# Kernel optimization log

Measured on AMD Instinct MI355X. Metric: run time of the kernel, lower is better.

Reference implementation:

```python
import jax, jax.numpy as jnp
import numpy as np

C_S, C_P, C_H, H, P_QK, P_V = 384, 128, 16, 12, 4, 8
B, N = 1, 512
INF = 1e5
EPS = 1e-8


def quat_to_rot(q):
    w, x, y, z = q[..., 0], q[..., 1], q[..., 2], q[..., 3]
    return jnp.stack([
        jnp.stack([1 - 2 * (y * y + z * z), 2 * (x * y - w * z), 2 * (x * z + w * y)], -1),
        jnp.stack([2 * (x * y + w * z), 1 - 2 * (x * x + z * z), 2 * (y * z - w * x)], -1),
        jnp.stack([2 * (x * z - w * y), 2 * (y * z + w * x), 1 - 2 * (x * x + y * y)], -1),
    ], -2)


def layer_norm(x, g, b):
    m = x.mean(-1, keepdims=True)
    v = ((x - m) ** 2).mean(-1, keepdims=True)
    return (x - m) * jax.lax.rsqrt(v + 1e-5) * g + b


def setup_inputs():
    key = jax.random.key(0)
    ks = iter(jax.random.split(key, 64))

    def w(shape, scale=0.02):
        return jax.random.normal(next(ks), shape, dtype=jnp.float32) * scale

    inp = {}
    inp['s'] = jax.random.normal(next(ks), (B, N, C_S), dtype=jnp.float32)
    inp['p'] = jax.random.normal(next(ks), (B, N, N, C_P), dtype=jnp.float32)
    q = jax.random.normal(next(ks), (B, N, 4), dtype=jnp.float32)
    inp['rot'] = quat_to_rot(q / jnp.linalg.norm(q, axis=-1, keepdims=True))
    inp['trans'] = jax.random.normal(next(ks), (B, N, 3), dtype=jnp.float32)
    inp['mask'] = jnp.ones((B, N), dtype=jnp.float32)
    inp['w_q'] = w((C_S, H * C_H)); inp['b_q'] = jnp.zeros((H * C_H,), jnp.float32)
    inp['w_kv'] = w((C_S, 2 * H * C_H)); inp['b_kv'] = jnp.zeros((2 * H * C_H,), jnp.float32)
    inp['w_qp'] = w((C_S, H * P_QK * 3)); inp['b_qp'] = jnp.zeros((H * P_QK * 3,), jnp.float32)
    inp['w_kvp'] = w((C_S, H * (P_QK + P_V) * 3)); inp['b_kvp'] = jnp.zeros((H * (P_QK + P_V) * 3,), jnp.float32)
    inp['w_b'] = w((C_P, H)); inp['b_b'] = jnp.zeros((H,), jnp.float32)
    inp['head_w'] = w((H,), 0.5)
    d_out = H * (C_H + C_P + P_V * 4)  # 2112
    inp['w_o'] = w((d_out, C_S)); inp['b_o'] = jnp.zeros((C_S,), jnp.float32)
    inp['ln1_g'] = jnp.ones((C_S,), jnp.float32); inp['ln1_b'] = jnp.zeros((C_S,), jnp.float32)
    for i in (1, 2, 3):
        inp['tw%d' % i] = w((C_S, C_S)); inp['tb%d' % i] = jnp.zeros((C_S,), jnp.float32)
    inp['ln2_g'] = jnp.ones((C_S,), jnp.float32); inp['ln2_b'] = jnp.zeros((C_S,), jnp.float32)
    inp['bb_w'] = w((C_S, 6)); inp['bb_b'] = jnp.zeros((6,), jnp.float32)
    return inp


def forward(s, p, rot, trans, mask, w_q, b_q, w_kv, b_kv, w_qp, b_qp, w_kvp, b_kvp,
            w_b, b_b, head_w, w_o, b_o, ln1_g, ln1_b,
            tw1, tb1, tw2, tb2, tw3, tb3, ln2_g, ln2_b, bb_w, bb_b):
    # ---- Invariant Point Attention ----
    q = (s @ w_q + b_q).reshape(B, N, H, C_H)
    k, v = jnp.split((s @ w_kv + b_kv).reshape(B, N, H, 2 * C_H), 2, axis=-1)
    qp = (s @ w_qp + b_qp).reshape(B, N, H * P_QK, 3)
    qp = (jnp.einsum('bnij,bnpj->bnpi', rot, qp) + trans[:, :, None, :]).reshape(B, N, H, P_QK, 3)
    kvp = (s @ w_kvp + b_kvp).reshape(B, N, H * (P_QK + P_V), 3)
    kvp = (jnp.einsum('bnij,bnpj->bnpi', rot, kvp) + trans[:, :, None, :]).reshape(B, N, H, P_QK + P_V, 3)
    kp, vp = kvp[..., :P_QK, :], kvp[..., P_QK:, :]
    bias = p @ w_b + b_b  # [B,N,N,H]
    a = jnp.einsum('bihc,bjhc->bhij', q, k) * float(np.sqrt(1.0 / (3 * C_H)))
    a = a + float(np.sqrt(1.0 / 3)) * jnp.transpose(bias, (0, 3, 1, 2))
    d2 = ((qp[:, :, None] - kp[:, None]) ** 2).sum(-1)  # [B,N,N,H,Pqk]
    hw = jax.nn.softplus(head_w) * float(np.sqrt(1.0 / (3 * (P_QK * 9.0 / 2))))
    pt_att = -0.5 * (d2 * hw[:, None]).sum(-1)  # [B,N,N,H]
    sq_mask = (mask[:, :, None] * mask[:, None, :] - 1.0) * INF  # [B,N,N]
    a = jax.nn.softmax(a + jnp.transpose(pt_att, (0, 3, 1, 2)) + sq_mask[:, None], axis=-1)
    o = jnp.einsum('bhij,bjhc->bihc', a, v).reshape(B, N, H * C_H)
    op = jnp.einsum('bhij,bjhpc->bihpc', a, vp) - trans[:, :, None, None, :]
    op = jnp.einsum('bnji,bnhpj->bnhpi', rot, op)  # invert-apply frames
    op_norm = jnp.sqrt((op ** 2).sum(-1) + EPS)  # [B,N,H,Pv]
    o_pair = jnp.einsum('bhij,bijc->bihc', a, p).reshape(B, N, H * C_P)
    cat = jnp.concatenate([o, op.reshape(B, N, H * P_V * 3), op_norm.reshape(B, N, H * P_V), o_pair], -1)
    s = s + cat @ w_o + b_o
    s = layer_norm(s, ln1_g, ln1_b)
    # ---- structure transition (1 layer, residual + LN) ----
    h = jax.nn.relu(s @ tw1 + tb1)
    h = jax.nn.relu(h @ tw2 + tb2)
    s = layer_norm(s + h @ tw3 + tb3, ln2_g, ln2_b)
    # ---- backbone update + frame compose ----
    upd = s @ bb_w + bb_b  # [B,N,6]
    quat = jnp.concatenate([jnp.ones((B, N, 1), s.dtype), upd[..., :3]], -1)
    quat = quat / jnp.linalg.norm(quat, axis=-1, keepdims=True)
    r_u = quat_to_rot(quat)
    rot_new = jnp.einsum('bnij,bnjk->bnik', rot, r_u)
    trans_new = jnp.einsum('bnij,bnj->bni', rot, upd[..., 3:]) + trans
    return s, rot_new, trans_new


def reference(s, p, rot, trans, mask, w_q, b_q, w_kv, b_kv, w_qp, b_qp, w_kvp, b_kvp,
              w_b, b_b, head_w, w_o, b_o, ln1_g, ln1_b,
              tw1, tb1, tw2, tb2, tw3, tb3, ln2_g, ln2_b, bb_w, bb_b):
    return forward(s, p, rot, trans, mask, w_q, b_q, w_kv, b_kv, w_qp, b_qp, w_kvp, b_kvp,
                   w_b, b_b, head_w, w_o, b_o, ln1_g, ln1_b,
                   tw1, tb1, tw2, tb2, tw3, tb3, ln2_g, ln2_b, bb_w, bb_b)
```

## Files before the change

### kernel.cpp

```cpp
#include <hip/hip_runtime.h>
#include <math.h>

#define N 512
#define CS 384
#define CP 128
#define CH 16
#define NH 12
#define NN (N*N)
#define DCAT 2112
#define INFV 100000.0f

__device__ __constant__ float SC_QK = 0.14433756729740643f;
#define SC_B  0.57735026918962576f
#define HW_SC 0.13608276348795434f

typedef __attribute__((ext_vector_type(8))) short bf16x8;
typedef __attribute__((ext_vector_type(4))) float f32x4;
typedef __attribute__((ext_vector_type(4))) short sh4;
typedef __attribute__((ext_vector_type(4))) unsigned u32x4;
typedef unsigned short ushort_t;

__device__ inline short f2bf(float v) {
    unsigned u = __builtin_bit_cast(unsigned, v);
    u += 0x7FFF + ((u >> 16) & 1);
    return (short)(u >> 16);
}
__device__ inline float bf2f(ushort_t u) {
    unsigned x = ((unsigned)u) << 16;
    return __builtin_bit_cast(float, x);
}
__device__ __forceinline__ unsigned cvtpk(float a, float b) {
    unsigned r;
    asm("v_cvt_pk_bf16_f32 %0, %1, %2" : "=v"(r) : "v"(a), "v"(b));
    return r;
}

__device__ __forceinline__ void gload16(const void* g, void* l) {
    __builtin_amdgcn_global_load_lds(
        (const __attribute__((address_space(1))) unsigned int*)g,
        (__attribute__((address_space(3))) unsigned int*)l,
        16, 0, 0);
}

struct PrepArgs {
    const float* wsrc0; const float* wsrc1; const float* wsrc2; const float* wsrc3;
    const float* wsrc4; const float* wsrc5; const float* wsrc6; const float* wsrc7;
    ushort_t* wdst0; ushort_t* wdst1; ushort_t* wdst2; ushort_t* wdst3;
    ushort_t* wdst4; ushort_t* wdst5; ushort_t* wdst6; ushort_t* wdst7;
    const float* s; ushort_t* sbf;
    const float* bq; const float* bkv; const float* bqp; const float* bkvp;
    float* biasp;
};

__global__ __launch_bounds__(256) void prep_kernel(PrepArgs a)
{
    const int b = blockIdx.x;
    if (b < 1668) {
        const float* src; ushort_t* dst; int begin, nx, Nc, K;
        if      (b < 72)   { src=a.wsrc0; dst=a.wdst0; begin=0;    nx=6;  Nc=192; K=384; }
        else if (b < 216)  { src=a.wsrc1; dst=a.wdst1; begin=72;   nx=12; Nc=384; K=384; }
        else if (b < 276)  { src=a.wsrc2; dst=a.wdst2; begin=216;  nx=5;  Nc=144; K=384; }
        else if (b < 444)  { src=a.wsrc3; dst=a.wdst3; begin=276;  nx=14; Nc=432; K=384; }
        else if (b < 1236) { src=a.wsrc4; dst=a.wdst4; begin=444;  nx=12; Nc=384; K=2112; }
        else if (b < 1380) { src=a.wsrc5; dst=a.wdst5; begin=1236; nx=12; Nc=384; K=384; }
        else if (b < 1524) { src=a.wsrc6; dst=a.wdst6; begin=1380; nx=12; Nc=384; K=384; }
        else               { src=a.wsrc7; dst=a.wdst7; begin=1524; nx=12; Nc=384; K=384; }
        int lb = b - begin;
        int cx = (lb % nx) * 32, ky = (lb / nx) * 32;
        __shared__ float tile[32][33];
        const int tx = threadIdx.x & 31, ty = threadIdx.x >> 5;
        for (int r = ty; r < 32; r += 8) {
            int c = cx + tx;
            tile[r][tx] = (c < Nc) ? src[(size_t)(ky + r) * Nc + c] : 0.f;
        }
        __syncthreads();
        for (int r = ty; r < 32; r += 8) {
            int orow = cx + r;
            if (orow < Nc)
                dst[(size_t)orow * K + ky + tx] = (ushort_t)f2bf(tile[tx][r]);
        }
    } else if (b < 1860) {
        int i4 = (b - 1668) * 256 + threadIdx.x;
        f32x4 v = *(const f32x4*)(a.s + (size_t)i4 * 4);
        sh4 o;
        o[0] = f2bf(v[0]); o[1] = f2bf(v[1]); o[2] = f2bf(v[2]); o[3] = f2bf(v[3]);
        *(sh4*)(a.sbf + (size_t)i4 * 4) = o;
    } else {
        for (int idx = threadIdx.x; idx < 1152; idx += 256) {
            float v;
            if (idx < 192)      v = a.bq[idx];
            else if (idx < 576) v = a.bkv[idx - 192];
            else if (idx < 720) v = a.bqp[idx - 576];
            else                v = a.bkvp[idx - 720];
            a.biasp[idx] = v;
        }
    }
}

__global__ __launch_bounds__(256) void gemm_bf16(
    const ushort_t* __restrict__ A, const ushort_t* __restrict__ Bt,
    float* __restrict__ part, int K, int KOUT, int nk)
{
    __shared__ __align__(16) ushort_t As[2][2048];
    __shared__ __align__(16) ushort_t Bs[2][2048];
    const int t = threadIdx.x, w = t >> 6, l = t & 63;
    const int i0 = blockIdx.x * 64, n0 = blockIdx.y * 64, sp = blockIdx.z;
    const int kbase = sp * nk * 32;

    const int srow = w * 16 + (l >> 2);
    const int skb = (l & 3) ^ ((srow >> 1) & 3);
    const ushort_t* aSrc = A + (size_t)(i0 + srow) * K + kbase + skb * 8;
    const ushort_t* bSrc = Bt + (size_t)(n0 + srow) * K + kbase + skb * 8;
    ushort_t* aDst = &As[0][0] + w * 512;
    ushort_t* bDst = &Bs[0][0] + w * 512;

    const int r0 = (w >> 1) * 32, c0 = (w & 1) * 32, lr = l & 15, hk = l >> 4;
    int aOff[2], bOff[2];
    #pragma unroll
    for (int m = 0; m < 2; ++m) {
        int row = r0 + m * 16 + lr;
        aOff[m] = row * 64 + ((hk ^ ((row >> 1) & 3)) << 4);
    }
    #pragma unroll
    for (int n = 0; n < 2; ++n) {
        int row = c0 + n * 16 + lr;
        bOff[n] = row * 64 + ((hk ^ ((row >> 1) & 3)) << 4);
    }

    f32x4 acc[2][2];
    #pragma unroll
    for (int m = 0; m < 2; ++m)
        #pragma unroll
        for (int n = 0; n < 2; ++n) acc[m][n] = (f32x4){0.f, 0.f, 0.f, 0.f};

    gload16(aSrc, aDst);
    gload16(bSrc, bDst);
    __syncthreads();

    int cur = 0;
    for (int it = 0; it < nk; ++it) {
        if (it + 1 < nk) {
            gload16(aSrc + (it + 1) * 32, aDst + (cur ^ 1) * 2048);
            gload16(bSrc + (it + 1) * 32, bDst + (cur ^ 1) * 2048);
        }
        const char* ab = (const char*)&As[cur][0];
        const char* bb = (const char*)&Bs[cur][0];
        bf16x8 a0 = *(const bf16x8*)(ab + aOff[0]);
        bf16x8 a1 = *(const bf16x8*)(ab + aOff[1]);
        bf16x8 b0 = *(const bf16x8*)(bb + bOff[0]);
        bf16x8 b1 = *(const bf16x8*)(bb + bOff[1]);
        acc[0][0] = __builtin_amdgcn_mfma_f32_16x16x32_bf16(a0, b0, acc[0][0], 0, 0, 0);
        acc[0][1] = __builtin_amdgcn_mfma_f32_16x16x32_bf16(a0, b1, acc[0][1], 0, 0, 0);
        acc[1][0] = __builtin_amdgcn_mfma_f32_16x16x32_bf16(a1, b0, acc[1][0], 0, 0, 0);
        acc[1][1] = __builtin_amdgcn_mfma_f32_16x16x32_bf16(a1, b1, acc[1][1], 0, 0, 0);
        __syncthreads();
        cur ^= 1;
    }

    #pragma unroll
    for (int m = 0; m < 2; ++m)
        #pragma unroll
        for (int n = 0; n < 2; ++n) {
            int col = n0 + c0 + n * 16 + lr;
            int rowb = i0 + r0 + m * 16 + (l >> 4) * 4;
            float* pr = part + ((size_t)sp * 512 + rowb) * KOUT + col;
            #pragma unroll
            for (int j = 0; j < 4; ++j)
                pr[(size_t)j * KOUT] = acc[m][n][j];
        }
}

__global__ void reduce_k(const float* __restrict__ parts, int S, int KOUT,
                         const float* __restrict__ bias, const float* __restrict__ resid,
                         int relu, float* __restrict__ outf, ushort_t* __restrict__ outbf)
{
    int i4 = blockIdx.x * 256 + threadIdx.x;
    int tot = 512 * KOUT / 4;
    if (i4 >= tot) return;
    int idx = i4 * 4, c = idx % KOUT;
    f32x4 v = *(const f32x4*)(bias + c);
    for (int s2 = 0; s2 < S; ++s2)
        v += *(const f32x4*)(parts + (size_t)s2 * 512 * KOUT + idx);
    if (resid) v += *(const f32x4*)(resid + idx);
    if (relu) {
        v[0] = fmaxf(v[0], 0.f); v[1] = fmaxf(v[1], 0.f);
        v[2] = fmaxf(v[2], 0.f); v[3] = fmaxf(v[3], 0.f);
    }
    if (outf) *(f32x4*)(outf + idx) = v;
    if (outbf) {
        sh4 o;
        o[0] = f2bf(v[0]); o[1] = f2bf(v[1]); o[2] = f2bf(v[2]); o[3] = f2bf(v[3]);
        *(sh4*)(outbf + idx) = o;
    }
}

__global__ void reduce_ln(const float* __restrict__ parts, int S,
                          const float* __restrict__ gbias, const float* __restrict__ resid,
                          const float* __restrict__ g, const float* __restrict__ b,
                          float* __restrict__ outf, ushort_t* __restrict__ outbf,
                          const float* __restrict__ bb_w, const float* __restrict__ bb_b,
                          const float* __restrict__ rot, const float* __restrict__ trans,
                          float* __restrict__ out_rot, float* __restrict__ out_trans)
{
    __shared__ float buf[384];
    __shared__ float red[2], red2[2];
    __shared__ float ush[2][6];
    const int i = blockIdx.x, t = threadIdx.x;
    float s = 0.f, sq = 0.f;
    for (int k = t; k < 384; k += 128) {
        float v = gbias[k] + resid[(size_t)i * 384 + k];
        for (int s2 = 0; s2 < S; ++s2)
            v += parts[((size_t)s2 * 512 + i) * 384 + k];
        buf[k] = v; s += v; sq += v * v;
    }
    for (int off = 32; off; off >>= 1) { s += __shfl_xor(s, off); sq += __shfl_xor(sq, off); }
    if ((t & 63) == 0) { red[t >> 6] = s; red2[t >> 6] = sq; }
    __syncthreads();
    float mean = (red[0] + red[1]) * (1.0f / 384.0f);
    float var = (red2[0] + red2[1]) * (1.0f / 384.0f) - mean * mean;
    float rstd = rsqrtf(var + 1e-5f);
    float onorm[3];
    #pragma unroll
    for (int kk = 0; kk < 3; ++kk) {
        int k = t + kk * 128;
        float o = (buf[k] - mean) * rstd * g[k] + b[k];
        onorm[kk] = o;
        if (outf) outf[(size_t)i * 384 + k] = o;
        if (outbf) outbf[(size_t)i * 384 + k] = (ushort_t)f2bf(o);
    }
    if (!bb_w) return;
    float u[6] = {0.f, 0.f, 0.f, 0.f, 0.f, 0.f};
    #pragma unroll
    for (int kk = 0; kk < 3; ++kk) {
        int k = t + kk * 128;
        float sv = onorm[kk];
        #pragma unroll
        for (int c = 0; c < 6; ++c) u[c] += sv * bb_w[k * 6 + c];
    }
    #pragma unroll
    for (int c = 0; c < 6; ++c)
        for (int off = 32; off; off >>= 1) u[c] += __shfl_xor(u[c], off);
    if ((t & 63) == 0) {
        #pragma unroll
        for (int c = 0; c < 6; ++c) ush[t >> 6][c] = u[c];
    }
    __syncthreads();
    if (t == 0) {
        float uu[6];
        #pragma unroll
        for (int c = 0; c < 6; ++c) uu[c] = ush[0][c] + ush[1][c] + bb_b[c];
        float inq = rsqrtf(1.0f + uu[0]*uu[0] + uu[1]*uu[1] + uu[2]*uu[2]);
        float w = inq, x = uu[0]*inq, y = uu[1]*inq, z = uu[2]*inq;
        float Ru[9];
        Ru[0] = 1.f - 2.f*(y*y + z*z); Ru[1] = 2.f*(x*y - w*z); Ru[2] = 2.f*(x*z + w*y);
        Ru[3] = 2.f*(x*y + w*z); Ru[4] = 1.f - 2.f*(x*x + z*z); Ru[5] = 2.f*(y*z - w*x);
        Ru[6] = 2.f*(x*z - w*y); Ru[7] = 2.f*(y*z + w*x); Ru[8] = 1.f - 2.f*(x*x + y*y);
        const float* R = rot + i * 9;
        #pragma unroll
        for (int a = 0; a < 3; ++a) {
            #pragma unroll
            for (int cc = 0; cc < 3; ++cc)
                out_rot[i * 9 + a * 3 + cc] =
                    R[a*3+0]*Ru[0+cc] + R[a*3+1]*Ru[3+cc] + R[a*3+2]*Ru[6+cc];
            out_trans[i * 3 + a] = R[a*3+0]*uu[3] + R[a*3+1]*uu[4] + R[a*3+2]*uu[5]
                                   + trans[i * 3 + a];
        }
    }
}

__global__ __launch_bounds__(256) void postproj_kernel(
    const float* __restrict__ parts, const float* __restrict__ biasp,
    const float* __restrict__ rot, const float* __restrict__ trans,
    const float* __restrict__ head_w, const float* __restrict__ mask,
    ushort_t* __restrict__ Qext, ushort_t* __restrict__ Kext, ushort_t* __restrict__ Vext)
{
    __shared__ float buf[1152];
    __shared__ float hwv[12], kc28[12];
    const int j = blockIdx.x, t = threadIdx.x;
    for (int c = t; c < 1152; c += 256)
        buf[c] = biasp[c] + parts[(size_t)j * 1152 + c] + parts[(size_t)(512 + j) * 1152 + c];
    if (t >= 192 && t < 204) {
        int h = t - 192;
        hwv[h] = HW_SC * log1pf(expf(head_w[h]));
    }
    __syncthreads();
    if (t < 192) {
        int base = 576 + t * 3;
        const float* R = rot + j * 9;
        const float* T = trans + j * 3;
        float x = buf[base], y = buf[base + 1], z = buf[base + 2];
        float nx = R[0]*x + R[1]*y + R[2]*z + T[0];
        float ny = R[3]*x + R[4]*y + R[5]*z + T[1];
        float nz = R[6]*x + R[7]*y + R[8]*z + T[2];
        buf[base] = nx; buf[base + 1] = ny; buf[base + 2] = nz;
    }
    __syncthreads();
    if (t < 12) {
        float s2 = 0.f;
        #pragma unroll
        for (int e = 0; e < 12; ++e) { float v = buf[720 + t * 36 + e]; s2 += v * v; }
        kc28[t] = -0.5f * hwv[t] * s2 + (mask[j] - 1.0f) * INFV;
    }
    __syncthreads();
    if (t < 192) {
        int h = t >> 4, c0 = (t & 15) * 2;
        float hwf = hwv[h];
        #pragma unroll
        for (int e = 0; e < 2; ++e) {
            int c = c0 + e;
            float qv, kv2;
            if (c < 16)      { qv = SC_QK * buf[h * 16 + c];           kv2 = buf[192 + h * 32 + c]; }
            else if (c < 28) { qv = hwf * buf[576 + h * 12 + (c - 16)]; kv2 = buf[720 + h * 36 + (c - 16)]; }
            else if (c == 28){ qv = 1.f;                               kv2 = kc28[h]; }
            else             { qv = 0.f;                               kv2 = 0.f; }
            Qext[(size_t)h * 16384 + j * 32 + c] = (ushort_t)f2bf(qv);
            Kext[(size_t)h * 16384 + j * 32 + c] = (ushort_t)f2bf(kv2);
        }
    }
    for (int idx = t; idx < 576; idx += 256) {
        int h = idx / 48, c = idx % 48;
        float v;
        if (c < 16)      v = buf[192 + h * 32 + 16 + c];
        else if (c < 40) v = buf[720 + h * 36 + 12 + (c - 16)];
        else             v = 0.f;
        Vext[(size_t)h * 24576 + c * 512 + j] = (ushort_t)f2bf(v);
    }
}

__global__ __launch_bounds__(256) void bias_mfma(
    const float* __restrict__ p, const float* __restrict__ w_b,
    const float* __restrict__ b_b, ushort_t* __restrict__ bias_b)
{
    __shared__ __align__(16) float Pf[64 * 128];
    __shared__ __align__(16) ushort_t Wbs[16 * 128];
    const int t = threadIdx.x, w = t >> 6;
    const size_t row0 = (size_t)blockIdx.x * 64;

    for (int idx = t; idx < 2048; idx += 256) {
        int h = idx >> 7, c = idx & 127;
        float v = (h < 12) ? w_b[c * 12 + h] : 0.f;
        int byte = h * 256 + ((c * 2) ^ ((h & 7) << 4));
        *(ushort_t*)((char*)Wbs + byte) = (ushort_t)f2bf(v);
    }
    #pragma unroll
    for (int k = 0; k < 8; ++k) {
        int s = k * 256 + t;
        int row = s >> 5, ch = s & 31;
        const char* src = (const char*)(p + (row0 + row) * 128) + ((ch ^ (row & 7)) * 16);
        gload16(src, (char*)Pf + (size_t)(k * 256 + w * 64) * 16);
    }
    __syncthreads();

    const int l = t & 63, lr = l & 15, hk = l >> 4;
    const int jb = w * 16;
    f32x4 acc = (f32x4){0.f, 0.f, 0.f, 0.f};
    #pragma unroll
    for (int ks = 0; ks < 4; ++ks) {
        int row = jb + lr;
        int kc = ks * 8 + hk * 2;
        const char* base = (const char*)Pf + row * 512;
        f32x4 v0 = *(const f32x4*)(base + ((kc ^ (row & 7)) * 16));
        f32x4 v1 = *(const f32x4*)(base + (((kc + 1) ^ (row & 7)) * 16));
        bf16x8 afr;
        afr[0] = f2bf(v0[0]); afr[1] = f2bf(v0[1]); afr[2] = f2bf(v0[2]); afr[3] = f2bf(v0[3]);
        afr[4] = f2bf(v1[0]); afr[5] = f2bf(v1[1]); afr[6] = f2bf(v1[2]); afr[7] = f2bf(v1[3]);
        bf16x8 bfr = *(const bf16x8*)((char*)Wbs + lr * 256 +
                        ((ks * 64 + hk * 16) ^ ((lr & 7) << 4)));
        acc = __builtin_amdgcn_mfma_f32_16x16x32_bf16(afr, bfr, acc, 0, 0, 0);
    }
    if (lr < 12) {
        float bb = b_b[lr];
        size_t gj = row0 + jb + hk * 4;
        sh4 o;
        #pragma unroll
        for (int r = 0; r < 4; ++r) o[r] = f2bf(SC_B * (acc[r] + bb));
        *(sh4*)(bias_b + (size_t)lr * NN + gj) = o;
    }
}

__global__ __launch_bounds__(256) void attn_mfma(
    const ushort_t* __restrict__ Qext, const ushort_t* __restrict__ Kext,
    const ushort_t* __restrict__ bias_b, const ushort_t* __restrict__ Vext,
    const float* __restrict__ rot, const float* __restrict__ trans,
    ushort_t* __restrict__ attn_b, ushort_t* __restrict__ catb)
{
    __shared__ float sc[16 * 516];
    __shared__ float redm[64];
    __shared__ float invr[16];
    __shared__ float opl[16][25];
    const int t = threadIdx.x, w = t >> 6, l = t & 63;
    const int i0 = blockIdx.x * 16, h = blockIdx.y;
    const int lr = l & 15, hk = l >> 4;

    #pragma unroll
    for (int it = 0; it < 8; ++it) {
        int elem = (t + it * 256) * 4;
        int i = elem >> 9, j = elem & 511;
        sh4 raw = *(const sh4*)(bias_b + (size_t)h * NN + (size_t)(i0 + i) * 512 + j);
        f32x4 v;
        v[0] = bf2f((ushort_t)raw[0]); v[1] = bf2f((ushort_t)raw[1]);
        v[2] = bf2f((ushort_t)raw[2]); v[3] = bf2f((ushort_t)raw[3]);
        *(f32x4*)(sc + i * 516 + j) = v;
    }
    __syncthreads();

    bf16x8 a0 = *(const bf16x8*)(Qext + (size_t)h * 16384 + (i0 + lr) * 32 + hk * 8);
    f32x4 acc[8];
    #pragma unroll
    for (int n = 0; n < 8; ++n) {
        bf16x8 b = *(const bf16x8*)(Kext + (size_t)h * 16384 +
                                    (w * 128 + n * 16 + lr) * 32 + hk * 8);
        acc[n] = __builtin_amdgcn_mfma_f32_16x16x32_bf16(a0, b, (f32x4){0.f,0.f,0.f,0.f}, 0, 0, 0);
    }

    float rmax[4] = {-3.0e38f, -3.0e38f, -3.0e38f, -3.0e38f};
    #pragma unroll
    for (int n = 0; n < 8; ++n) {
        int col = w * 128 + n * 16 + lr;
        #pragma unroll
        for (int r = 0; r < 4; ++r) {
            int row = hk * 4 + r;
            float v = acc[n][r] + sc[row * 516 + col];
            sc[row * 516 + col] = v;
            rmax[r] = fmaxf(rmax[r], v);
        }
    }
    #pragma unroll
    for (int r = 0; r < 4; ++r) {
        float v = rmax[r];
        v = fmaxf(v, __shfl_xor(v, 1));
        v = fmaxf(v, __shfl_xor(v, 2));
        v = fmaxf(v, __shfl_xor(v, 4));
        v = fmaxf(v, __shfl_xor(v, 8));
        if (lr == 0) redm[w * 16 + hk * 4 + r] = v;
    }
    __syncthreads();

    {
        int row = t >> 4, g = t & 15;
        float mx = fmaxf(fmaxf(redm[row], redm[16 + row]),
                         fmaxf(redm[32 + row], redm[48 + row]));
        float sum = 0.f;
        float* sr = sc + row * 516;
        for (int c = g; c < 512; c += 16) {
            float e = expf(sr[c] - mx);
            sr[c] = e;
            sum += e;
        }
        sum += __shfl_xor(sum, 1);
        sum += __shfl_xor(sum, 2);
        sum += __shfl_xor(sum, 4);
        sum += __shfl_xor(sum, 8);
        if (g == 0) invr[row] = 1.0f / sum;
    }
    __syncthreads();

    #pragma unroll
    for (int it = 0; it < 8; ++it) {
        int elem = (t + it * 256) * 4;
        int i = elem >> 9, j = elem & 511;
        f32x4 v = *(const f32x4*)(sc + i * 516 + j);
        float iv = invr[i];
        sh4 o;
        o[0] = f2bf(v[0] * iv); o[1] = f2bf(v[1] * iv);
        o[2] = f2bf(v[2] * iv); o[3] = f2bf(v[3] * iv);
        *(sh4*)(attn_b + (size_t)h * NN + (size_t)(i0 + i) * 512 + j) = o;
    }

    f32x4 acc3[3];
    acc3[0] = (f32x4){0.f,0.f,0.f,0.f};
    acc3[1] = (f32x4){0.f,0.f,0.f,0.f};
    acc3[2] = (f32x4){0.f,0.f,0.f,0.f};
    const ushort_t* vbase = Vext + (size_t)h * 24576 + lr * 512 + hk * 8;
    #pragma unroll
    for (int kt = 0; kt < 16; ++kt) {
        const float* srow = sc + lr * 516 + kt * 32 + hk * 8;
        f32x4 x0 = *(const f32x4*)(srow);
        f32x4 x1 = *(const f32x4*)(srow + 4);
        u32x4 ap;
        ap[0] = cvtpk(x0[0], x0[1]); ap[1] = cvtpk(x0[2], x0[3]);
        ap[2] = cvtpk(x1[0], x1[1]); ap[3] = cvtpk(x1[2], x1[3]);
        bf16x8 af = __builtin_bit_cast(bf16x8, ap);
        #pragma unroll
        for (int n = 0; n < 3; ++n) {
            bf16x8 bf = *(const bf16x8*)(vbase + n * 16 * 512 + kt * 32);
            acc3[n] = __builtin_amdgcn_mfma_f32_16x16x32_bf16(af, bf, acc3[n], 0, 0, 0);
        }
    }
    #pragma unroll
    for (int n = 0; n < 3; ++n) {
        int c = n * 16 + lr;
        #pragma unroll
        for (int r = 0; r < 4; ++r) {
            int ri = hk * 4 + r;
            float val = acc3[n][r] * invr[ri];
            if (c < 16)
                catb[(size_t)(i0 + ri) * DCAT + h * 16 + c] = (ushort_t)f2bf(val);
            else if (c < 40)
                opl[ri][c - 16] = val;
        }
    }
    __syncthreads();
    if (t < 128) {
        int i16 = t >> 3, pv = t & 7;
        int i = i0 + i16;
        const float* T = trans + i * 3;
        const float* R = rot + i * 9;
        float x = opl[i16][pv * 3 + 0] - T[0];
        float y = opl[i16][pv * 3 + 1] - T[1];
        float z = opl[i16][pv * 3 + 2] - T[2];
        float rx = R[0] * x + R[3] * y + R[6] * z;
        float ry = R[1] * x + R[4] * y + R[7] * z;
        float rz = R[2] * x + R[5] * y + R[8] * z;
        float nm = sqrtf(rx * rx + ry * ry + rz * rz + 1e-8f);
        ushort_t* cr = catb + (size_t)i * DCAT;
        cr[192 + h * 24 + pv * 3 + 0] = (ushort_t)f2bf(rx);
        cr[192 + h * 24 + pv * 3 + 1] = (ushort_t)f2bf(ry);
        cr[192 + h * 24 + pv * 3 + 2] = (ushort_t)f2bf(rz);
        cr[480 + h * 8 + pv] = (ushort_t)f2bf(nm);
    }
}

__global__ __launch_bounds__(256) void opair_mfma(
    const ushort_t* __restrict__ attn_b, const float* __restrict__ p,
    ushort_t* __restrict__ catb)
{
    __shared__ __align__(16) ushort_t As2[16 * 512];
    __shared__ __align__(16) ushort_t Pt[2][128 * 72];
    const int t = threadIdx.x, i = blockIdx.x;
    const int w = t >> 6, l = t & 63;
    const int lr = l & 15, hk = l >> 4;

    #pragma unroll
    for (int ii = 0; ii < 4; ++ii) {
        int idx = (t + ii * 256) * 8;
        int h = idx >> 9, j = idx & 511;
        bf16x8 v;
        if (h < 12) v = *(const bf16x8*)(attn_b + (size_t)h * NN + (size_t)i * 512 + j);
        else        v = (bf16x8){0,0,0,0,0,0,0,0};
        *(bf16x8*)((char*)As2 + h * 1024 + ((j * 2) ^ ((h & 7) << 4))) = v;
    }

    const int jA = (t >> 3) * 2;
    const int c0 = (t & 7) * 16;
    const float* psrc = p + (size_t)i * 65536;

    f32x4 va[4], vb[4];
    #pragma unroll
    for (int q = 0; q < 4; ++q) {
        va[q] = *(const f32x4*)(psrc + (size_t)jA * 128 + c0 + q * 4);
        vb[q] = *(const f32x4*)(psrc + (size_t)(jA + 1) * 128 + c0 + q * 4);
    }

    #define PACK_TILE(buf)                                                       \
        {                                                                        \
            ushort_t* ptw = &Pt[buf][0];                                         \
            _Pragma("unroll")                                                    \
            for (int e = 0; e < 16; ++e) {                                       \
                int c = c0 + e;                                                  \
                unsigned pk = cvtpk(va[e >> 2][e & 3], vb[e >> 2][e & 3]);       \
                int byte = c * 144 + ((jA * 2) ^ (((c >> 4) & 7) << 4));         \
                *(unsigned*)((char*)ptw + byte) = pk;                            \
            }                                                                    \
        }
    #define LOAD_TILE(tile)                                                      \
        {                                                                        \
            const float* s0 = psrc + (size_t)((tile) * 64 + jA) * 128 + c0;      \
            _Pragma("unroll")                                                    \
            for (int q = 0; q < 4; ++q) {                                        \
                va[q] = *(const f32x4*)(s0 + q * 4);                             \
                vb[q] = *(const f32x4*)(s0 + 128 + q * 4);                       \
            }                                                                    \
        }

    PACK_TILE(0);
    LOAD_TILE(1);

    f32x4 acc[2];
    acc[0] = (f32x4){0.f, 0.f, 0.f, 0.f};
    acc[1] = (f32x4){0.f, 0.f, 0.f, 0.f};

    int cur = 0;
    for (int tile = 0; tile < 8; ++tile) {
        __syncthreads();
        const char* pt = (const char*)&Pt[cur][0];
        #pragma unroll
        for (int ks = 0; ks < 2; ++ks) {
            bf16x8 afr = *(const bf16x8*)((char*)As2 + lr * 1024 +
                            ((tile * 128 + ks * 64 + hk * 16) ^ ((lr & 7) << 4)));
            #pragma unroll
            for (int n = 0; n < 2; ++n) {
                int c = w * 32 + n * 16 + lr;
                bf16x8 bfr = *(const bf16x8*)(pt + c * 144 +
                                ((ks * 64 + hk * 16) ^ (((c >> 4) & 7) << 4)));
                acc[n] = __builtin_amdgcn_mfma_f32_16x16x32_bf16(afr, bfr, acc[n], 0, 0, 0);
            }
        }
        if (tile < 7) {
            PACK_TILE(cur ^ 1);
            if (tile < 6) LOAD_TILE(tile + 2);
            cur ^= 1;
        }
    }
    #undef PACK_TILE
    #undef LOAD_TILE
    #pragma unroll
    for (int n = 0; n < 2; ++n) {
        int c = w * 32 + n * 16 + lr;
        #pragma unroll
        for (int r = 0; r < 4; ++r) {
            int h = hk * 4 + r;
            if (h < 12)
                catb[(size_t)i * DCAT + 576 + h * 128 + c] = (ushort_t)f2bf(acc[n][r]);
        }
    }
}

extern "C" void kernel_launch(void* const* d_in, const int* in_sizes, int n_in,
                              void* d_out, int out_size, void* d_ws, size_t ws_size,
                              hipStream_t stream)
{
    const float* s      = (const float*)d_in[0];
    const float* p      = (const float*)d_in[1];
    const float* rot    = (const float*)d_in[2];
    const float* trans  = (const float*)d_in[3];
    const float* mask   = (const float*)d_in[4];
    const float* w_q    = (const float*)d_in[5];
    const float* b_q    = (const float*)d_in[6];
    const float* w_kv   = (const float*)d_in[7];
    const float* b_kv   = (const float*)d_in[8];
    const float* w_qp   = (const float*)d_in[9];
    const float* b_qp   = (const float*)d_in[10];
    const float* w_kvp  = (const float*)d_in[11];
    const float* b_kvp  = (const float*)d_in[12];
    const float* w_b    = (const float*)d_in[13];
    const float* b_b    = (const float*)d_in[14];
    const float* head_w = (const float*)d_in[15];
    const float* w_o    = (const float*)d_in[16];
    const float* b_o    = (const float*)d_in[17];
    const float* ln1_g  = (const float*)d_in[18];
    const float* ln1_b  = (const float*)d_in[19];
    const float* tw1    = (const float*)d_in[20];
    const float* tb1    = (const float*)d_in[21];
    const float* tw2    = (const float*)d_in[22];
    const float* tb2    = (const float*)d_in[23];
    const float* tw3    = (const float*)d_in[24];
    const float* tb3    = (const float*)d_in[25];
    const float* ln2_g  = (const float*)d_in[26];
    const float* ln2_b  = (const float*)d_in[27];
    const float* bb_w   = (const float*)d_in[28];
    const float* bb_b   = (const float*)d_in[29];

    float* ws = (float*)d_ws;
    float*    parts = ws;
    float*    s1    = parts + 1179648;
    float*    biasp = s1 + 196608;
    ushort_t* ub     = (ushort_t*)(biasp + 1152);
    ushort_t* bias_b = ub;
    ushort_t* attn_b = bias_b + 3145728;
    ushort_t* catb   = attn_b + 3145728;
    ushort_t* sbf    = catb + 1081344;
    ushort_t* s1bf   = sbf + 196608;
    ushort_t* h1bf   = s1bf + 196608;
    ushort_t* h2bf   = h1bf + 196608;
    ushort_t* Qext   = h2bf + 196608;
    ushort_t* Kext   = Qext + 196608;
    ushort_t* Vext   = Kext + 196608;
    ushort_t* Wtp    = Vext + 294912;
    ushort_t* Wto    = Wtp + 442368;
    ushort_t* Wt1    = Wto + 811008;
    ushort_t* Wt2    = Wt1 + 147456;
    ushort_t* Wt3    = Wt2 + 147456;

    float* out_s     = (float*)d_out;
    float* out_rot   = out_s + 196608;
    float* out_trans = out_rot + 4608;

    PrepArgs pa;
    pa.wsrc0 = w_q;  pa.wdst0 = Wtp;
    pa.wsrc1 = w_kv; pa.wdst1 = Wtp + (size_t)192 * 384;
    pa.wsrc2 = w_qp; pa.wdst2 = Wtp + (size_t)576 * 384;
    pa.wsrc3 = w_kvp; pa.wdst3 = Wtp + (size_t)720 * 384;
    pa.wsrc4 = w_o;  pa.wdst4 = Wto;
    pa.wsrc5 = tw1;  pa.wdst5 = Wt1;
    pa.wsrc6 = tw2;  pa.wdst6 = Wt2;
    pa.wsrc7 = tw3;  pa.wdst7 = Wt3;
    pa.s = s; pa.sbf = sbf;
    pa.bq = b_q; pa.bkv = b_kv; pa.bqp = b_qp; pa.bkvp = b_kvp;
    pa.biasp = biasp;
    prep_kernel<<<1861, 256, 0, stream>>>(pa);

    gemm_bf16<<<dim3(8, 18, 2), 256, 0, stream>>>(sbf, Wtp, parts, 384, 1152, 6);
    postproj_kernel<<<512, 256, 0, stream>>>(parts, biasp, rot, trans, head_w, mask,
                                             Qext, Kext, Vext);

    bias_mfma<<<4096, 256, 0, stream>>>(p, w_b, b_b, bias_b);
    attn_mfma<<<dim3(32, 12), 256, 0, stream>>>(Qext, Kext, bias_b, Vext, rot, trans,
                                                attn_b, catb);
    opair_mfma<<<512, 256, 0, stream>>>(attn_b, p, catb);

    gemm_bf16<<<dim3(8, 6, 6), 256, 0, stream>>>(catb, Wto, parts, 2112, 384, 11);
    reduce_ln<<<512, 128, 0, stream>>>(parts, 6, b_o, s, ln1_g, ln1_b, s1, s1bf,
                                       nullptr, nullptr, nullptr, nullptr, nullptr, nullptr);

    gemm_bf16<<<dim3(8, 6, 3), 256, 0, stream>>>(s1bf, Wt1, parts, 384, 384, 4);
    reduce_k<<<192, 256, 0, stream>>>(parts, 3, 384, tb1, nullptr, 1, nullptr, h1bf);
    gemm_bf16<<<dim3(8, 6, 3), 256, 0, stream>>>(h1bf, Wt2, parts, 384, 384, 4);
    reduce_k<<<192, 256, 0, stream>>>(parts, 3, 384, tb2, nullptr, 1, nullptr, h2bf);
    gemm_bf16<<<dim3(8, 6, 3), 256, 0, stream>>>(h2bf, Wt3, parts, 384, 384, 4);
    reduce_ln<<<512, 128, 0, stream>>>(parts, 3, tb3, s1, ln2_g, ln2_b, out_s, nullptr,
                                       bb_w, bb_b, rot, trans, out_rot, out_trans);
}
```

Measured before the change: 129.1 us.

## Fuse LN1, three-layer transition MLP, LN2 and frame update into one kernel

Replaces the eight-launch tail (reduce_ln, three split-K GEMMs with reduce kernels, final reduce_ln plus backbone update) with one kernel. Each of 64 blocks owns 8 rows, keeps activations in swizzled LDS as bf16, and runs the 384x384 matmuls with MFMA, reading weights straight from global memory. This removes launch overhead and the round trips of partial sums through global memory. In exchange only 64 blocks are active, half of each 16-row MFMA tile is padding, and every block re-reads all three weight matrices.

```diff
diff --git a/kernel.cpp b/kernel.cpp
--- a/kernel.cpp
+++ b/kernel.cpp
@@ -170,104 +170,6 @@
         }
 }
 
-__global__ void reduce_k(const float* __restrict__ parts, int S, int KOUT,
-                         const float* __restrict__ bias, const float* __restrict__ resid,
-                         int relu, float* __restrict__ outf, ushort_t* __restrict__ outbf)
-{
-    int i4 = blockIdx.x * 256 + threadIdx.x;
-    int tot = 512 * KOUT / 4;
-    if (i4 >= tot) return;
-    int idx = i4 * 4, c = idx % KOUT;
-    f32x4 v = *(const f32x4*)(bias + c);
-    for (int s2 = 0; s2 < S; ++s2)
-        v += *(const f32x4*)(parts + (size_t)s2 * 512 * KOUT + idx);
-    if (resid) v += *(const f32x4*)(resid + idx);
-    if (relu) {
-        v[0] = fmaxf(v[0], 0.f); v[1] = fmaxf(v[1], 0.f);
-        v[2] = fmaxf(v[2], 0.f); v[3] = fmaxf(v[3], 0.f);
-    }
-    if (outf) *(f32x4*)(outf + idx) = v;
-    if (outbf) {
-        sh4 o;
-        o[0] = f2bf(v[0]); o[1] = f2bf(v[1]); o[2] = f2bf(v[2]); o[3] = f2bf(v[3]);
-        *(sh4*)(outbf + idx) = o;
-    }
-}
-
-__global__ void reduce_ln(const float* __restrict__ parts, int S,
-                          const float* __restrict__ gbias, const float* __restrict__ resid,
-                          const float* __restrict__ g, const float* __restrict__ b,
-                          float* __restrict__ outf, ushort_t* __restrict__ outbf,
-                          const float* __restrict__ bb_w, const float* __restrict__ bb_b,
-                          const float* __restrict__ rot, const float* __restrict__ trans,
-                          float* __restrict__ out_rot, float* __restrict__ out_trans)
-{
-    __shared__ float buf[384];
-    __shared__ float red[2], red2[2];
-    __shared__ float ush[2][6];
-    const int i = blockIdx.x, t = threadIdx.x;
-    float s = 0.f, sq = 0.f;
-    for (int k = t; k < 384; k += 128) {
-        float v = gbias[k] + resid[(size_t)i * 384 + k];
-        for (int s2 = 0; s2 < S; ++s2)
-            v += parts[((size_t)s2 * 512 + i) * 384 + k];
-        buf[k] = v; s += v; sq += v * v;
-    }
-    for (int off = 32; off; off >>= 1) { s += __shfl_xor(s, off); sq += __shfl_xor(sq, off); }
-    if ((t & 63) == 0) { red[t >> 6] = s; red2[t >> 6] = sq; }
-    __syncthreads();
-    float mean = (red[0] + red[1]) * (1.0f / 384.0f);
-    float var = (red2[0] + red2[1]) * (1.0f / 384.0f) - mean * mean;
-    float rstd = rsqrtf(var + 1e-5f);
-    float onorm[3];
-    #pragma unroll
-    for (int kk = 0; kk < 3; ++kk) {
-        int k = t + kk * 128;
-        float o = (buf[k] - mean) * rstd * g[k] + b[k];
-        onorm[kk] = o;
-        if (outf) outf[(size_t)i * 384 + k] = o;
-        if (outbf) outbf[(size_t)i * 384 + k] = (ushort_t)f2bf(o);
-    }
-    if (!bb_w) return;
-    float u[6] = {0.f, 0.f, 0.f, 0.f, 0.f, 0.f};
-    #pragma unroll
-    for (int kk = 0; kk < 3; ++kk) {
-        int k = t + kk * 128;
-        float sv = onorm[kk];
-        #pragma unroll
-        for (int c = 0; c < 6; ++c) u[c] += sv * bb_w[k * 6 + c];
-    }
-    #pragma unroll
-    for (int c = 0; c < 6; ++c)
-        for (int off = 32; off; off >>= 1) u[c] += __shfl_xor(u[c], off);
-    if ((t & 63) == 0) {
-        #pragma unroll
-        for (int c = 0; c < 6; ++c) ush[t >> 6][c] = u[c];
-    }
-    __syncthreads();
-    if (t == 0) {
-        float uu[6];
-        #pragma unroll
-        for (int c = 0; c < 6; ++c) uu[c] = ush[0][c] + ush[1][c] + bb_b[c];
-        float inq = rsqrtf(1.0f + uu[0]*uu[0] + uu[1]*uu[1] + uu[2]*uu[2]);
-        float w = inq, x = uu[0]*inq, y = uu[1]*inq, z = uu[2]*inq;
-        float Ru[9];
-        Ru[0] = 1.f - 2.f*(y*y + z*z); Ru[1] = 2.f*(x*y - w*z); Ru[2] = 2.f*(x*z + w*y);
-        Ru[3] = 2.f*(x*y + w*z); Ru[4] = 1.f - 2.f*(x*x + z*z); Ru[5] = 2.f*(y*z - w*x);
-        Ru[6] = 2.f*(x*z - w*y); Ru[7] = 2.f*(y*z + w*x); Ru[8] = 1.f - 2.f*(x*x + y*y);
-        const float* R = rot + i * 9;
-        #pragma unroll
-        for (int a = 0; a < 3; ++a) {
-            #pragma unroll
-            for (int cc = 0; cc < 3; ++cc)
-                out_rot[i * 9 + a * 3 + cc] =
-                    R[a*3+0]*Ru[0+cc] + R[a*3+1]*Ru[3+cc] + R[a*3+2]*Ru[6+cc];
-            out_trans[i * 3 + a] = R[a*3+0]*uu[3] + R[a*3+1]*uu[4] + R[a*3+2]*uu[5]
-                                   + trans[i * 3 + a];
-        }
-    }
-}
-
 __global__ __launch_bounds__(256) void postproj_kernel(
     const float* __restrict__ parts, const float* __restrict__ biasp,
     const float* __restrict__ rot, const float* __restrict__ trans,
@@ -612,6 +514,166 @@
             int h = hk * 4 + r;
             if (h < 12)
                 catb[(size_t)i * DCAT + 576 + h * 128 + c] = (ushort_t)f2bf(acc[n][r]);
+        }
+    }
+}
+
+__global__ __launch_bounds__(256) void tailrows_kernel(
+    const float* __restrict__ parts, const float* __restrict__ b_o,
+    const float* __restrict__ s,
+    const float* __restrict__ ln1_g, const float* __restrict__ ln1_b,
+    const ushort_t* __restrict__ Wt1, const float* __restrict__ tb1,
+    const ushort_t* __restrict__ Wt2, const float* __restrict__ tb2,
+    const ushort_t* __restrict__ Wt3, const float* __restrict__ tb3,
+    const float* __restrict__ ln2_g, const float* __restrict__ ln2_b,
+    const float* __restrict__ bb_w, const float* __restrict__ bb_b,
+    const float* __restrict__ rot, const float* __restrict__ trans,
+    float* __restrict__ out_s, float* __restrict__ out_rot, float* __restrict__ out_trans)
+{
+    __shared__ __align__(16) ushort_t Abuf[2][16 * 384];
+    __shared__ float s1f[8 * 384];
+    __shared__ float s2f[8 * 384];
+    const int t = threadIdx.x;
+    const int i0 = blockIdx.x * 8;
+    const int w = t >> 6, l = t & 63, lr = l & 15, hk = l >> 4;
+
+    for (int k = t; k < 16 * 384; k += 256) { Abuf[0][k] = 0; Abuf[1][k] = 0; }
+    __syncthreads();
+
+    {
+        const int r = t >> 5, g = t & 31;
+        float vals[12];
+        float sum = 0.f, sq = 0.f;
+        #pragma unroll
+        for (int kk = 0; kk < 12; ++kk) {
+            int k = g + kk * 32;
+            float v = b_o[k] + s[(size_t)(i0 + r) * 384 + k];
+            #pragma unroll
+            for (int sp = 0; sp < 6; ++sp)
+                v += parts[(size_t)sp * 196608 + (size_t)(i0 + r) * 384 + k];
+            vals[kk] = v; sum += v; sq += v * v;
+        }
+        #pragma unroll
+        for (int off = 16; off; off >>= 1) {
+            sum += __shfl_xor(sum, off); sq += __shfl_xor(sq, off);
+        }
+        float mean = sum * (1.0f / 384.0f);
+        float var = sq * (1.0f / 384.0f) - mean * mean;
+        float rstd = rsqrtf(var + 1e-5f);
+        #pragma unroll
+        for (int kk = 0; kk < 12; ++kk) {
+            int k = g + kk * 32;
+            float o = (vals[kk] - mean) * rstd * ln1_g[k] + ln1_b[k];
+            s1f[r * 384 + k] = o;
+            int byte = r * 768 + ((k * 2) ^ ((r & 7) << 4));
+            *(ushort_t*)((char*)&Abuf[0][0] + byte) = (ushort_t)f2bf(o);
+        }
+    }
+    __syncthreads();
+
+    #pragma unroll 1
+    for (int layer = 0; layer < 3; ++layer) {
+        const ushort_t* Wt = (layer == 0) ? Wt1 : (layer == 1) ? Wt2 : Wt3;
+        const float* bias = (layer == 0) ? tb1 : (layer == 1) ? tb2 : tb3;
+        const ushort_t* Ain = &Abuf[layer & 1][0];
+        ushort_t* Aout = &Abuf[(layer & 1) ^ 1][0];
+
+        f32x4 acc[6];
+        #pragma unroll
+        for (int f = 0; f < 6; ++f) acc[f] = (f32x4){0.f, 0.f, 0.f, 0.f};
+        #pragma unroll
+        for (int ks = 0; ks < 12; ++ks) {
+            int abyte = lr * 768 + (((ks * 32 + hk * 8) * 2) ^ ((lr & 7) << 4));
+            bf16x8 a = *(const bf16x8*)((const char*)Ain + abyte);
+            #pragma unroll
+            for (int f = 0; f < 6; ++f) {
+                int col = w * 96 + f * 16 + lr;
+                bf16x8 b = *(const bf16x8*)(Wt + (size_t)col * 384 + ks * 32 + hk * 8);
+                acc[f] = __builtin_amdgcn_mfma_f32_16x16x32_bf16(a, b, acc[f], 0, 0, 0);
+            }
+        }
+        if (layer < 2) {
+            #pragma unroll
+            for (int f = 0; f < 6; ++f) {
+                int col = w * 96 + f * 16 + lr;
+                float bv = bias[col];
+                #pragma unroll
+                for (int r = 0; r < 4; ++r) {
+                    int row = hk * 4 + r;
+                    if (row < 8) {
+                        float o = fmaxf(acc[f][r] + bv, 0.f);
+                        int byte = row * 768 + ((col * 2) ^ ((row & 7) << 4));
+                        *(ushort_t*)((char*)Aout + byte) = (ushort_t)f2bf(o);
+                    }
+                }
+            }
+        } else {
+            #pragma unroll
+            for (int f = 0; f < 6; ++f) {
+                int col = w * 96 + f * 16 + lr;
+                float bv = bias[col];
+                #pragma unroll
+                for (int r = 0; r < 4; ++r) {
+                    int row = hk * 4 + r;
+                    if (row < 8)
+                        s2f[row * 384 + col] = acc[f][r] + bv + s1f[row * 384 + col];
+                }
+            }
+        }
+        __syncthreads();
+    }
+
+    {
+        const int r = t >> 5, g = t & 31;
+        float vals[12];
+        float sum = 0.f, sq = 0.f;
+        #pragma unroll
+        for (int kk = 0; kk < 12; ++kk) {
+            float v = s2f[r * 384 + g + kk * 32];
+            vals[kk] = v; sum += v; sq += v * v;
+        }
+        #pragma unroll
+        for (int off = 16; off; off >>= 1) {
+            sum += __shfl_xor(sum, off); sq += __shfl_xor(sq, off);
+        }
+        float mean = sum * (1.0f / 384.0f);
+        float var = sq * (1.0f / 384.0f) - mean * mean;
+        float rstd = rsqrtf(var + 1e-5f);
+        float u[6] = {0.f, 0.f, 0.f, 0.f, 0.f, 0.f};
+        #pragma unroll
+        for (int kk = 0; kk < 12; ++kk) {
+            int k = g + kk * 32;
+            float o = (vals[kk] - mean) * rstd * ln2_g[k] + ln2_b[k];
+            out_s[(size_t)(i0 + r) * 384 + k] = o;
+            #pragma unroll
+            for (int c = 0; c < 6; ++c) u[c] += o * bb_w[k * 6 + c];
+        }
+        #pragma unroll
+        for (int c = 0; c < 6; ++c) {
+            #pragma unroll
+            for (int off = 16; off; off >>= 1) u[c] += __shfl_xor(u[c], off);
+        }
+        if (g == 0) {
+            int i = i0 + r;
+            float uu[6];
+            #pragma unroll
+            for (int c = 0; c < 6; ++c) uu[c] = u[c] + bb_b[c];
+            float inq = rsqrtf(1.0f + uu[0]*uu[0] + uu[1]*uu[1] + uu[2]*uu[2]);
+            float qw = inq, x = uu[0]*inq, y = uu[1]*inq, z = uu[2]*inq;
+            float Ru[9];
+            Ru[0] = 1.f - 2.f*(y*y + z*z); Ru[1] = 2.f*(x*y - qw*z); Ru[2] = 2.f*(x*z + qw*y);
+            Ru[3] = 2.f*(x*y + qw*z); Ru[4] = 1.f - 2.f*(x*x + z*z); Ru[5] = 2.f*(y*z - qw*x);
+            Ru[6] = 2.f*(x*z - qw*y); Ru[7] = 2.f*(y*z + qw*x); Ru[8] = 1.f - 2.f*(x*x + y*y);
+            const float* R = rot + i * 9;
+            #pragma unroll
+            for (int a = 0; a < 3; ++a) {
+                #pragma unroll
+                for (int cc = 0; cc < 3; ++cc)
+                    out_rot[i * 9 + a * 3 + cc] =
+                        R[a*3+0]*Ru[0+cc] + R[a*3+1]*Ru[3+cc] + R[a*3+2]*Ru[6+cc];
+                out_trans[i * 3 + a] = R[a*3+0]*uu[3] + R[a*3+1]*uu[4] + R[a*3+2]*uu[5]
+                                       + trans[i * 3 + a];
+            }
         }
     }
 }
@@ -700,14 +762,8 @@
     opair_mfma<<<512, 256, 0, stream>>>(attn_b, p, catb);
 
     gemm_bf16<<<dim3(8, 6, 6), 256, 0, stream>>>(catb, Wto, parts, 2112, 384, 11);
-    reduce_ln<<<512, 128, 0, stream>>>(parts, 6, b_o, s, ln1_g, ln1_b, s1, s1bf,
-                                       nullptr, nullptr, nullptr, nullptr, nullptr, nullptr);
-
-    gemm_bf16<<<dim3(8, 6, 3), 256, 0, stream>>>(s1bf, Wt1, parts, 384, 384, 4);
-    reduce_k<<<192, 256, 0, stream>>>(parts, 3, 384, tb1, nullptr, 1, nullptr, h1bf);
-    gemm_bf16<<<dim3(8, 6, 3), 256, 0, stream>>>(h1bf, Wt2, parts, 384, 384, 4);
-    reduce_k<<<192, 256, 0, stream>>>(parts, 3, 384, tb2, nullptr, 1, nullptr, h2bf);
-    gemm_bf16<<<dim3(8, 6, 3), 256, 0, stream>>>(h2bf, Wt3, parts, 384, 384, 4);
-    reduce_ln<<<512, 128, 0, stream>>>(parts, 3, tb3, s1, ln2_g, ln2_b, out_s, nullptr,
-                                       bb_w, bb_b, rot, trans, out_rot, out_trans);
-}
+    tailrows_kernel<<<64, 256, 0, stream>>>(parts, b_o, s, ln1_g, ln1_b,
+                                            Wt1, tb1, Wt2, tb2, Wt3, tb3,
+                                            ln2_g, ln2_b, bb_w, bb_b, rot, trans,
+                                            out_s, out_rot, out_trans);
+}
```

After: 136.1 us. 1.05x slower.
